# Kernel tuning notes

Hardware: AMD Instinct MI355X
Metric: run time of the kernel (lower is better)

Reference implementation:

```python
import jax, jax.numpy as jnp
import numpy as np

M, N, B, L = 512, 2048, 4, 20
H_DENSITY = 0.02  # Tanner graph sparsity: row weight ~N*p=40, col weight ~M*p=10


def setup_inputs() -> dict:
    key = jax.random.key(0)
    ks = jax.random.split(key, 10)
    H = jax.random.bernoulli(ks[0], H_DENSITY, (M, N)).astype(jnp.float32)
    llrs = jax.random.uniform(ks[1], (N,), jnp.float32)
    syndromes = jax.random.randint(ks[2], (B, M, 1), 0, 2, jnp.int32)
    errors = jax.random.randint(ks[3], (B, N), 0, 2, jnp.int32)
    weights_de = jax.random.uniform(ks[4], (L, M, N), jnp.float32)
    weights_llr = jax.random.uniform(ks[5], (L, N), jnp.float32)
    marg_weights_de = jax.random.uniform(ks[6], (L, M, N), jnp.float32)
    marg_weights_llr = jax.random.uniform(ks[7], (L, N), jnp.float32)
    rhos = jnp.ones((L,), jnp.float32)
    residual_weights = jnp.zeros((L,), jnp.float32)
    return dict(syndromes=syndromes, errors=errors, H=H, llrs=llrs,
                weights_de=weights_de, weights_llr=weights_llr,
                marg_weights_de=marg_weights_de, marg_weights_llr=marg_weights_llr,
                rhos=rhos, residual_weights=residual_weights)


def reference(syndromes, errors, H, llrs, weights_de, weights_llr,
              marg_weights_de, marg_weights_llr, rhos, residual_weights):
    batch = syndromes.shape[0]
    m, n = H.shape
    rhos_norm = jax.nn.softmax(rhos)                       # (L,)
    sign = 1.0 - 2.0 * syndromes.astype(H.dtype)           # (B,m,1): (-1)**syndrome
    err_f = errors.astype(H.dtype)                         # (B,n)
    eps = 1e-6

    def step(msgs_dn, xs):
        w_de, w_llr, mw_de, mw_llr, rho, rw = xs
        # error-node (variable) update: column-sum minus self, masked by H
        msgs_en = (H * (llrs * w_llr)
                   + jnp.sum(msgs_dn * w_de, axis=1, keepdims=True)) * H - msgs_dn
        # detector-node (check) update: tanh-product rule with self-exclusion
        d = jnp.tanh(msgs_en * 0.5)
        d = jnp.where(d == 0, jnp.asarray(1.0, d.dtype), d)
        d = jnp.clip(d, -1.0 + eps, 1.0 - eps)
        row_prod = jnp.prod(d, axis=2, keepdims=True)      # (B,m,1)
        msgs_new = 2.0 * jnp.arctanh(row_prod / d) * (sign * H) + rw * msgs_dn
        # marginal beliefs and weighted BCE loss
        beliefs = jnp.sum(msgs_new * mw_de, axis=1) + llrs * mw_llr   # (B,n)
        loss_b = jnp.sum(jax.nn.softplus(beliefs) - (1.0 - err_f) * beliefs, axis=1)
        return msgs_new, rho * loss_b

    init = jnp.zeros((batch, m, n), H.dtype)
    _, losses = jax.lax.scan(
        step, init,
        (weights_de, weights_llr, marg_weights_de, marg_weights_llr,
         rhos_norm, residual_weights))
    return jnp.sum(losses) / batch
```

## Files before the change

### kernel.cpp

```cpp
#include <hip/hip_runtime.h>

#define MM 512
#define NN 2048
#define BB 4
#define LL 20
#define MAXDEG 128
#define EMAX  24576
#define NT    1024
#define RR    8
#define ROWSB 64
#define SLOTS 4096
#define COLSB 256
#define EPSV  1e-6f

#define WS_ROW_DEG   0
#define WS_ROW_PAD   2048
#define WS_ROW_OFFF  264192
#define WS_ROW_PTR   266240
#define WS_EDGE_CSR  268416
#define WS_WDE_P     366720
#define WS_MWDE_P    2988160
#define WS_COLPART   5609600
#define WS_BELPART   6133888
#define WS_BAR       6658176

__global__ __launch_bounds__(64)
void build_rows(const float* __restrict__ H, int* __restrict__ row_deg,
                int* __restrict__ row_pad, float* __restrict__ row_offf) {
    int i = blockIdx.x, lane = threadIdx.x;
    const float* hrow = H + (size_t)i * NN;
    float v[32];
    #pragma unroll
    for (int c = 0; c < 32; ++c) v[c] = hrow[c * 64 + lane];
    int base = 0;
    #pragma unroll
    for (int c = 0; c < 32; ++c) {
        bool pred = v[c] != 0.0f;
        unsigned long long mask = __ballot(pred);
        int before = __popcll(mask & ((1ull << lane) - 1ull));
        if (pred) {
            int k = base + before;
            if (k < MAXDEG) row_pad[i * MAXDEG + k] = c * 64 + lane;
        }
        base += __popcll(mask);
    }
    if (lane == 0) {
        row_deg[i] = base < MAXDEG ? base : MAXDEG;
        row_offf[i] = powf(1.0f - EPSV, (float)(NN - base));
    }
}

__global__ __launch_bounds__(512)
void scan_rows(const int* __restrict__ row_deg, int* __restrict__ row_ptr) {
    __shared__ int tmp[512];
    int t = threadIdx.x;
    tmp[t] = row_deg[t];
    __syncthreads();
    for (int off = 1; off < 512; off <<= 1) {
        int v = (t >= off) ? tmp[t - off] : 0;
        __syncthreads();
        tmp[t] += v;
        __syncthreads();
    }
    if (t == 0) row_ptr[0] = 0;
    row_ptr[t + 1] = tmp[t];
}

__global__ __launch_bounds__(64)
void fill_csr(const int* __restrict__ row_deg, const int* __restrict__ row_pad,
              const int* __restrict__ row_ptr, unsigned* __restrict__ edge_csr) {
    int i = blockIdx.x, lane = threadIdx.x;
    int deg = row_deg[i], base = row_ptr[i];
    for (int k = lane; k < deg; k += 64)
        edge_csr[base + k] = ((unsigned)i << 16) | (unsigned)row_pad[i * MAXDEG + k];
}

__global__ __launch_bounds__(256)
void gather_weights(const float* __restrict__ w_de, const float* __restrict__ mw_de,
                    const unsigned* __restrict__ edge_csr, const int* __restrict__ row_ptr,
                    float* __restrict__ wde_p, float* __restrict__ mwde_p) {
    int idx = blockIdx.x * 256 + threadIdx.x;
    int l = idx / (RR * SLOTS);
    int rem = idx - l * (RR * SLOTS);
    int r = rem / SLOTS, s = rem - r * SLOTS;
    int e = row_ptr[r * ROWSB] + s;
    if (e < row_ptr[(r + 1) * ROWSB]) {
        unsigned pk = edge_csr[e];
        size_t src = (size_t)l * MM * NN + (size_t)(pk >> 16) * NN + (pk & 0xffffu);
        wde_p[idx]  = w_de[src];
        mwde_p[idx] = mw_de[src];
    } else {
        wde_p[idx]  = 0.0f;
        mwde_p[idx] = 0.0f;
    }
}

__device__ __forceinline__ void grid_barrier(int* ctr) {
    __syncthreads();
    if (threadIdx.x == 0) {
        asm volatile("s_waitcnt vmcnt(0)" ::: "memory");
        __hip_atomic_fetch_add(ctr, 1, __ATOMIC_RELAXED, __HIP_MEMORY_SCOPE_AGENT);
        int it = 0;
        while (__hip_atomic_load(ctr, __ATOMIC_RELAXED, __HIP_MEMORY_SCOPE_AGENT) < RR) {
            __builtin_amdgcn_s_sleep(1);
            if (++it > (1 << 22)) break;
        }
        asm volatile("" ::: "memory");
    }
    __syncthreads();
}

__global__ __launch_bounds__(NT, 4)
void nbp_main(const int* __restrict__ synd, const int* __restrict__ errs,
              const float* __restrict__ llrs,
              const float* __restrict__ w_llr, const float* __restrict__ mw_llr,
              const float* __restrict__ rhos, const float* __restrict__ resw,
              const int* __restrict__ row_ptr, const float* __restrict__ row_offf,
              const unsigned* __restrict__ edge_csr,
              const float* __restrict__ wde_p, const float* __restrict__ mwde_p,
              float* __restrict__ colpart, float* __restrict__ belpart,
              int* __restrict__ bar, float* __restrict__ out) {
    __shared__ float d_sb[SLOTS];
    __shared__ float colsum_s[NN];
    __shared__ float bel_s[NN];
    __shared__ float ncs_s[NN];
    __shared__ float llrs_s[NN];
    __shared__ float rowprod_s[ROWSB];
    __shared__ float rp_coef[ROWSB];
    __shared__ int   rowptr_s[ROWSB + 1];
    __shared__ float rho_n[LL];
    __shared__ float red[16];

    const int blk = blockIdx.x;
    const int b = blk & 3, r = blk >> 2;
    const int i0 = r * ROWSB;
    const int tid = threadIdx.x;
    const int lane = tid & 63, wave = tid >> 6;

    int* bar_b = bar + b * 64;

    if (tid == 0) {
        float mx = -1e30f;
        for (int l = 0; l < LL; ++l) mx = fmaxf(mx, rhos[l]);
        float s = 0.0f;
        for (int l = 0; l < LL; ++l) { float e = __expf(rhos[l] - mx); rho_n[l] = e; s += e; }
        for (int l = 0; l < LL; ++l) rho_n[l] /= s;
    }
    if (tid < ROWSB) {
        int i = i0 + tid;
        rowptr_s[tid] = row_ptr[i];
        rp_coef[tid] = row_offf[i] * (1.0f - 2.0f * (float)synd[b * MM + i]);
    }
    if (tid == ROWSB) rowptr_s[ROWSB] = row_ptr[i0 + ROWSB];
    for (int j = tid; j < NN; j += NT) {
        float lj = llrs[j];
        llrs_s[j] = lj;
        colsum_s[j] = lj * w_llr[j];
    }

    const int e_lo = row_ptr[i0], e_hi = row_ptr[i0 + ROWSB];
    const int cnt = e_hi - e_lo;
    const int s0 = 4 * tid;

    unsigned idx[4];
    float msg[4], d_r[4];
    #pragma unroll
    for (int k = 0; k < 4; ++k) {
        int e = e_lo + s0 + k;
        idx[k] = edge_csr[(s0 + k) < cnt ? e : e_lo] - ((unsigned)i0 << 16);
        msg[k] = 0.0f;
    }
    __syncthreads();

    float loss = 0.0f;

    for (int l = 0; l < LL; ++l) {
        const float rw = resw[l];
        const int par = l & 1;
        float* colpart_b = colpart + ((size_t)par * BB + b) * RR * NN;
        float* belpart_b = belpart + ((size_t)par * BB + b) * RR * NN;

        const float4 mq = *(const float4*)(mwde_p + ((size_t)(l * RR + r) * SLOTS) + s0);
        float4 wq = make_float4(0.f, 0.f, 0.f, 0.f);
        if (l + 1 < LL)
            wq = *(const float4*)(wde_p + ((size_t)((l + 1) * RR + r) * SLOTS) + s0);
        const float mv[4] = {mq.x, mq.y, mq.z, mq.w};
        const float wn[4] = {wq.x, wq.y, wq.z, wq.w};

        #pragma unroll
        for (int k = 0; k < 4; ++k) {
            int j = idx[k] & 0xffffu;
            float en = colsum_s[j] - msg[k];
            float t = __expf(en);
            float d = 1.0f - 2.0f * __builtin_amdgcn_rcpf(t + 1.0f);
            if (d == 0.0f) d = 1.0f;
            d = fminf(fmaxf(d, -1.0f + EPSV), 1.0f - EPSV);
            d_r[k] = d;
        }
        *(float4*)&d_sb[s0] = make_float4(d_r[0], d_r[1], d_r[2], d_r[3]);
        __syncthreads();

        if (tid < 4 * ROWSB) {
            int i = tid >> 2, q = tid & 3;
            int s = rowptr_s[i] - e_lo;
            int deg = rowptr_s[i + 1] - rowptr_s[i];
            float p = 1.0f;
            for (int c = q; c < deg; c += 4) p *= d_sb[s + c];
            p *= __shfl_xor(p, 1);
            p *= __shfl_xor(p, 2);
            if (q == 0) rowprod_s[i] = p * rp_coef[i];
        } else {
            for (int j = tid - 4 * ROWSB; j < NN; j += NT - 4 * ROWSB) {
                bel_s[j] = 0.0f;
                ncs_s[j] = 0.0f;
            }
        }
        __syncthreads();

        #pragma unroll
        for (int k = 0; k < 4; ++k) {
            int il = idx[k] >> 16;
            int j  = idx[k] & 0xffffu;
            float rq = rowprod_s[il] * __builtin_amdgcn_rcpf(d_r[k]);
            float v = __logf(1.0f + rq) - __logf(1.0f - rq) + rw * msg[k];
            msg[k] = v;
            if (s0 + k < cnt) {
                atomicAdd(&bel_s[j], v * mv[k]);
                if (l + 1 < LL) atomicAdd(&ncs_s[j], v * wn[k]);
            }
        }
        __syncthreads();
        for (int j = tid; j < NN; j += NT) {
            __hip_atomic_store(&belpart_b[r * NN + j], bel_s[j],
                               __ATOMIC_RELAXED, __HIP_MEMORY_SCOPE_AGENT);
            __hip_atomic_store(&colpart_b[r * NN + j], ncs_s[j],
                               __ATOMIC_RELAXED, __HIP_MEMORY_SCOPE_AGENT);
        }
        grid_barrier(&bar_b[l]);

        if (tid < COLSB) {
            int j = r * COLSB + tid;
            float bel = llrs_s[j] * mw_llr[l * NN + j];
            float* bp = belpart_b + j;
            #pragma unroll
            for (int r2 = 0; r2 < RR; ++r2)
                bel += __hip_atomic_load(&bp[r2 * NN],
                                         __ATOMIC_RELAXED, __HIP_MEMORY_SCOPE_AGENT);
            float sp = fmaxf(bel, 0.0f) + log1pf(__expf(-fabsf(bel)));
            loss += rho_n[l] * (sp - (1.0f - (float)errs[b * NN + j]) * bel);
        }
        if (l + 1 < LL) {
            const float* wl_next = w_llr + (l + 1) * NN;
            for (int j = tid; j < NN; j += NT) {
                float s = llrs_s[j] * wl_next[j];
                float* cp = colpart_b + j;
                #pragma unroll
                for (int r2 = 0; r2 < RR; ++r2)
                    s += __hip_atomic_load(&cp[r2 * NN],
                                           __ATOMIC_RELAXED, __HIP_MEMORY_SCOPE_AGENT);
                colsum_s[j] = s;
            }
        }
        __syncthreads();
    }

    #pragma unroll
    for (int off = 32; off > 0; off >>= 1) loss += __shfl_down(loss, off);
    if (lane == 0) red[wave] = loss;
    __syncthreads();
    if (wave == 0) {
        float v = (lane < 16) ? red[lane] : 0.0f;
        #pragma unroll
        for (int off = 8; off > 0; off >>= 1) v += __shfl_down(v, off);
        if (lane == 0) atomicAdd(out, v * 0.25f);
    }
}

extern "C" void kernel_launch(void* const* d_in, const int* in_sizes, int n_in,
                              void* d_out, int out_size, void* d_ws, size_t ws_size,
                              hipStream_t stream) {
    const int*   synd  = (const int*)  d_in[0];
    const int*   errs  = (const int*)  d_in[1];
    const float* H     = (const float*)d_in[2];
    const float* llrs  = (const float*)d_in[3];
    const float* w_de  = (const float*)d_in[4];
    const float* w_llr = (const float*)d_in[5];
    const float* mw_de = (const float*)d_in[6];
    const float* mw_llr= (const float*)d_in[7];
    const float* rhos  = (const float*)d_in[8];
    const float* resw  = (const float*)d_in[9];

    char* ws = (char*)d_ws;
    int*      row_deg  = (int*)     (ws + WS_ROW_DEG);
    int*      row_pad  = (int*)     (ws + WS_ROW_PAD);
    float*    row_offf = (float*)   (ws + WS_ROW_OFFF);
    int*      row_ptr  = (int*)     (ws + WS_ROW_PTR);
    unsigned* edge_csr = (unsigned*)(ws + WS_EDGE_CSR);
    float*    wde_p    = (float*)   (ws + WS_WDE_P);
    float*    mwde_p   = (float*)   (ws + WS_MWDE_P);
    float*    colpart  = (float*)   (ws + WS_COLPART);
    float*    belpart  = (float*)   (ws + WS_BELPART);
    int*      bar      = (int*)     (ws + WS_BAR);
    float*    out      = (float*)d_out;

    hipMemsetAsync(bar, 0, BB * 64 * sizeof(int), stream);
    hipMemsetAsync(d_out, 0, sizeof(float), stream);

    build_rows<<<MM, 64, 0, stream>>>(H, row_deg, row_pad, row_offf);
    scan_rows<<<1, 512, 0, stream>>>(row_deg, row_ptr);
    fill_csr<<<MM, 64, 0, stream>>>(row_deg, row_pad, row_ptr, edge_csr);
    gather_weights<<<(LL * RR * SLOTS) / 256, 256, 0, stream>>>(w_de, mw_de, edge_csr,
                                                                row_ptr, wde_p, mwde_p);
    nbp_main<<<BB * RR, NT, 0, stream>>>(synd, errs, llrs, w_llr, mw_llr, rhos, resw,
                                         row_ptr, row_offf, edge_csr, wde_p, mwde_p,
                                         colpart, belpart, bar, out);
}
```

Before: 424.7 us.

## Partition edges by column slices instead of row blocks to shrink cross-block exchange

Each of the 8 blocks per batch now owns a 256-column slice of the edges instead of a 64-row slice. Column sums and beliefs become block-local, so the only cross-block exchange per layer is 512 partial row products per slice, down from two full 2048-wide column partial arrays. The setup now needs count, scan and fill passes per slice, and rows are reduced serially per thread. The grid barrier moves to between the row-product phase and the message update.

```diff
diff --git a/kernel.cpp b/kernel.cpp
--- a/kernel.cpp
+++ b/kernel.cpp
@@ -5,24 +5,22 @@
 #define BB 4
 #define LL 20
 #define MAXDEG 128
-#define EMAX  24576
 #define NT    1024
 #define RR    8
-#define ROWSB 64
+#define COLSB 256
 #define SLOTS 4096
-#define COLSB 256
 #define EPSV  1e-6f
 
 #define WS_ROW_DEG   0
 #define WS_ROW_PAD   2048
 #define WS_ROW_OFFF  264192
-#define WS_ROW_PTR   266240
-#define WS_EDGE_CSR  268416
-#define WS_WDE_P     366720
-#define WS_MWDE_P    2988160
-#define WS_COLPART   5609600
-#define WS_BELPART   6133888
-#define WS_BAR       6658176
+#define WS_DEG_RB    266240
+#define WS_RPTR_RB   282624
+#define WS_EDGE_CS   299040
+#define WS_WDE_P     430112
+#define WS_MWDE_P    3051552
+#define WS_PP        5672992
+#define WS_BAR       5804064
 
 __global__ __launch_bounds__(64)
 void build_rows(const float* __restrict__ H, int* __restrict__ row_deg,
@@ -51,10 +49,26 @@
 }
 
 __global__ __launch_bounds__(512)
-void scan_rows(const int* __restrict__ row_deg, int* __restrict__ row_ptr) {
+void count_slices(const int* __restrict__ row_deg, const int* __restrict__ row_pad,
+                  int* __restrict__ deg_rb) {
+    int i = threadIdx.x;
+    int deg = row_deg[i];
+    int cnt[RR];
+    #pragma unroll
+    for (int r = 0; r < RR; ++r) cnt[r] = 0;
+    for (int k = 0; k < deg; ++k) {
+        int c = row_pad[i * MAXDEG + k];
+        cnt[c >> 8]++;
+    }
+    #pragma unroll
+    for (int r = 0; r < RR; ++r) deg_rb[r * MM + i] = cnt[r];
+}
+
+__global__ __launch_bounds__(512)
+void scan_slices(const int* __restrict__ deg_rb, int* __restrict__ rptr_rb) {
     __shared__ int tmp[512];
-    int t = threadIdx.x;
-    tmp[t] = row_deg[t];
+    int r = blockIdx.x, t = threadIdx.x;
+    tmp[t] = deg_rb[r * MM + t];
     __syncthreads();
     for (int off = 1; off < 512; off <<= 1) {
         int v = (t >= off) ? tmp[t - off] : 0;
@@ -62,30 +76,39 @@
         tmp[t] += v;
         __syncthreads();
     }
-    if (t == 0) row_ptr[0] = 0;
-    row_ptr[t + 1] = tmp[t];
-}
-
-__global__ __launch_bounds__(64)
-void fill_csr(const int* __restrict__ row_deg, const int* __restrict__ row_pad,
-              const int* __restrict__ row_ptr, unsigned* __restrict__ edge_csr) {
-    int i = blockIdx.x, lane = threadIdx.x;
-    int deg = row_deg[i], base = row_ptr[i];
-    for (int k = lane; k < deg; k += 64)
-        edge_csr[base + k] = ((unsigned)i << 16) | (unsigned)row_pad[i * MAXDEG + k];
+    if (t == 0) rptr_rb[r * 513] = 0;
+    rptr_rb[r * 513 + t + 1] = tmp[t];
+}
+
+__global__ __launch_bounds__(512)
+void fill_cs(const int* __restrict__ row_deg, const int* __restrict__ row_pad,
+             const int* __restrict__ rptr_rb, unsigned* __restrict__ edge_cs) {
+    int i = threadIdx.x;
+    int deg = row_deg[i];
+    int cnt[RR];
+    #pragma unroll
+    for (int r = 0; r < RR; ++r) cnt[r] = 0;
+    for (int k = 0; k < deg; ++k) {
+        int c = row_pad[i * MAXDEG + k];
+        int r = c >> 8;
+        int pos = rptr_rb[r * 513 + i] + cnt[r]++;
+        if (pos < SLOTS)
+            edge_cs[r * SLOTS + pos] = ((unsigned)i << 16) | (unsigned)c;
+    }
 }
 
 __global__ __launch_bounds__(256)
 void gather_weights(const float* __restrict__ w_de, const float* __restrict__ mw_de,
-                    const unsigned* __restrict__ edge_csr, const int* __restrict__ row_ptr,
+                    const unsigned* __restrict__ edge_cs, const int* __restrict__ rptr_rb,
                     float* __restrict__ wde_p, float* __restrict__ mwde_p) {
     int idx = blockIdx.x * 256 + threadIdx.x;
     int l = idx / (RR * SLOTS);
     int rem = idx - l * (RR * SLOTS);
     int r = rem / SLOTS, s = rem - r * SLOTS;
-    int e = row_ptr[r * ROWSB] + s;
-    if (e < row_ptr[(r + 1) * ROWSB]) {
-        unsigned pk = edge_csr[e];
+    int tot = rptr_rb[r * 513 + MM];
+    if (tot > SLOTS) tot = SLOTS;
+    if (s < tot) {
+        unsigned pk = edge_cs[r * SLOTS + s];
         size_t src = (size_t)l * MM * NN + (size_t)(pk >> 16) * NN + (pk & 0xffffu);
         wde_p[idx]  = w_de[src];
         mwde_p[idx] = mw_de[src];
@@ -115,25 +138,25 @@
               const float* __restrict__ llrs,
               const float* __restrict__ w_llr, const float* __restrict__ mw_llr,
               const float* __restrict__ rhos, const float* __restrict__ resw,
-              const int* __restrict__ row_ptr, const float* __restrict__ row_offf,
-              const unsigned* __restrict__ edge_csr,
+              const int* __restrict__ rptr_rb, const float* __restrict__ row_offf,
+              const unsigned* __restrict__ edge_cs,
               const float* __restrict__ wde_p, const float* __restrict__ mwde_p,
-              float* __restrict__ colpart, float* __restrict__ belpart,
-              int* __restrict__ bar, float* __restrict__ out) {
+              float* __restrict__ pp, int* __restrict__ bar,
+              float* __restrict__ out) {
     __shared__ float d_sb[SLOTS];
-    __shared__ float colsum_s[NN];
-    __shared__ float bel_s[NN];
-    __shared__ float ncs_s[NN];
-    __shared__ float llrs_s[NN];
-    __shared__ float rowprod_s[ROWSB];
-    __shared__ float rp_coef[ROWSB];
-    __shared__ int   rowptr_s[ROWSB + 1];
+    __shared__ float colsum_s[COLSB];
+    __shared__ float bel_s[COLSB];
+    __shared__ float ncs_s[COLSB];
+    __shared__ float llrs_s[COLSB];
+    __shared__ float ef_s[COLSB];
+    __shared__ float rowprod_s[MM];
+    __shared__ float rp_coef[MM];
+    __shared__ int   rowptr_s[MM + 1];
     __shared__ float rho_n[LL];
     __shared__ float red[16];
 
     const int blk = blockIdx.x;
     const int b = blk & 3, r = blk >> 2;
-    const int i0 = r * ROWSB;
     const int tid = threadIdx.x;
     const int lane = tid & 63, wave = tid >> 6;
 
@@ -146,28 +169,31 @@
         for (int l = 0; l < LL; ++l) { float e = __expf(rhos[l] - mx); rho_n[l] = e; s += e; }
         for (int l = 0; l < LL; ++l) rho_n[l] /= s;
     }
-    if (tid < ROWSB) {
-        int i = i0 + tid;
-        rowptr_s[tid] = row_ptr[i];
-        rp_coef[tid] = row_offf[i] * (1.0f - 2.0f * (float)synd[b * MM + i]);
-    }
-    if (tid == ROWSB) rowptr_s[ROWSB] = row_ptr[i0 + ROWSB];
-    for (int j = tid; j < NN; j += NT) {
+    if (tid < MM) {
+        rowptr_s[tid] = rptr_rb[r * 513 + tid];
+        rp_coef[tid] = row_offf[tid] * (1.0f - 2.0f * (float)synd[b * MM + tid]);
+    }
+    if (tid == MM) rowptr_s[MM] = rptr_rb[r * 513 + MM];
+    if (tid < COLSB) {
+        int j = r * COLSB + tid;
         float lj = llrs[j];
-        llrs_s[j] = lj;
-        colsum_s[j] = lj * w_llr[j];
-    }
-
-    const int e_lo = row_ptr[i0], e_hi = row_ptr[i0 + ROWSB];
-    const int cnt = e_hi - e_lo;
+        llrs_s[tid] = lj;
+        colsum_s[tid] = lj * w_llr[j];
+        ef_s[tid] = 1.0f - (float)errs[b * NN + j];
+        bel_s[tid] = 0.0f;
+        ncs_s[tid] = 0.0f;
+    }
+
+    int cnt = rptr_rb[r * 513 + MM];
+    if (cnt > SLOTS) cnt = SLOTS;
     const int s0 = 4 * tid;
 
     unsigned idx[4];
     float msg[4], d_r[4];
     #pragma unroll
     for (int k = 0; k < 4; ++k) {
-        int e = e_lo + s0 + k;
-        idx[k] = edge_csr[(s0 + k) < cnt ? e : e_lo] - ((unsigned)i0 << 16);
+        int e = r * SLOTS + s0 + k;
+        idx[k] = edge_cs[(s0 + k) < cnt ? e : r * SLOTS];
         msg[k] = 0.0f;
     }
     __syncthreads();
@@ -177,8 +203,7 @@
     for (int l = 0; l < LL; ++l) {
         const float rw = resw[l];
         const int par = l & 1;
-        float* colpart_b = colpart + ((size_t)par * BB + b) * RR * NN;
-        float* belpart_b = belpart + ((size_t)par * BB + b) * RR * NN;
+        float* pp_b = pp + ((size_t)par * BB + b) * RR * MM;
 
         const float4 mq = *(const float4*)(mwde_p + ((size_t)(l * RR + r) * SLOTS) + s0);
         float4 wq = make_float4(0.f, 0.f, 0.f, 0.f);
@@ -189,8 +214,8 @@
 
         #pragma unroll
         for (int k = 0; k < 4; ++k) {
-            int j = idx[k] & 0xffffu;
-            float en = colsum_s[j] - msg[k];
+            int jl = idx[k] & 255u;
+            float en = colsum_s[jl] - msg[k];
             float t = __expf(en);
             float d = 1.0f - 2.0f * __builtin_amdgcn_rcpf(t + 1.0f);
             if (d == 0.0f) d = 1.0f;
@@ -200,65 +225,49 @@
         *(float4*)&d_sb[s0] = make_float4(d_r[0], d_r[1], d_r[2], d_r[3]);
         __syncthreads();
 
-        if (tid < 4 * ROWSB) {
-            int i = tid >> 2, q = tid & 3;
-            int s = rowptr_s[i] - e_lo;
-            int deg = rowptr_s[i + 1] - rowptr_s[i];
+        if (tid < MM) {
+            int lo = rowptr_s[tid], hi = rowptr_s[tid + 1];
+            if (hi > SLOTS) hi = SLOTS;
             float p = 1.0f;
-            for (int c = q; c < deg; c += 4) p *= d_sb[s + c];
-            p *= __shfl_xor(p, 1);
-            p *= __shfl_xor(p, 2);
-            if (q == 0) rowprod_s[i] = p * rp_coef[i];
-        } else {
-            for (int j = tid - 4 * ROWSB; j < NN; j += NT - 4 * ROWSB) {
-                bel_s[j] = 0.0f;
-                ncs_s[j] = 0.0f;
-            }
+            for (int s = lo; s < hi; ++s) p *= d_sb[s];
+            __hip_atomic_store(&pp_b[r * MM + tid], p,
+                               __ATOMIC_RELAXED, __HIP_MEMORY_SCOPE_AGENT);
+        }
+        grid_barrier(&bar_b[l]);
+
+        if (tid < MM) {
+            float p = rp_coef[tid];
+            #pragma unroll
+            for (int r2 = 0; r2 < RR; ++r2)
+                p *= __hip_atomic_load(&pp_b[r2 * MM + tid],
+                                       __ATOMIC_RELAXED, __HIP_MEMORY_SCOPE_AGENT);
+            rowprod_s[tid] = p;
         }
         __syncthreads();
 
         #pragma unroll
         for (int k = 0; k < 4; ++k) {
             int il = idx[k] >> 16;
-            int j  = idx[k] & 0xffffu;
+            int jl = idx[k] & 255u;
             float rq = rowprod_s[il] * __builtin_amdgcn_rcpf(d_r[k]);
             float v = __logf(1.0f + rq) - __logf(1.0f - rq) + rw * msg[k];
             msg[k] = v;
             if (s0 + k < cnt) {
-                atomicAdd(&bel_s[j], v * mv[k]);
-                if (l + 1 < LL) atomicAdd(&ncs_s[j], v * wn[k]);
+                atomicAdd(&bel_s[jl], v * mv[k]);
+                if (l + 1 < LL) atomicAdd(&ncs_s[jl], v * wn[k]);
             }
         }
         __syncthreads();
-        for (int j = tid; j < NN; j += NT) {
-            __hip_atomic_store(&belpart_b[r * NN + j], bel_s[j],
-                               __ATOMIC_RELAXED, __HIP_MEMORY_SCOPE_AGENT);
-            __hip_atomic_store(&colpart_b[r * NN + j], ncs_s[j],
-                               __ATOMIC_RELAXED, __HIP_MEMORY_SCOPE_AGENT);
-        }
-        grid_barrier(&bar_b[l]);
 
         if (tid < COLSB) {
             int j = r * COLSB + tid;
-            float bel = llrs_s[j] * mw_llr[l * NN + j];
-            float* bp = belpart_b + j;
-            #pragma unroll
-            for (int r2 = 0; r2 < RR; ++r2)
-                bel += __hip_atomic_load(&bp[r2 * NN],
-                                         __ATOMIC_RELAXED, __HIP_MEMORY_SCOPE_AGENT);
+            float bel = llrs_s[tid] * mw_llr[l * NN + j] + bel_s[tid];
+            bel_s[tid] = 0.0f;
             float sp = fmaxf(bel, 0.0f) + log1pf(__expf(-fabsf(bel)));
-            loss += rho_n[l] * (sp - (1.0f - (float)errs[b * NN + j]) * bel);
-        }
-        if (l + 1 < LL) {
-            const float* wl_next = w_llr + (l + 1) * NN;
-            for (int j = tid; j < NN; j += NT) {
-                float s = llrs_s[j] * wl_next[j];
-                float* cp = colpart_b + j;
-                #pragma unroll
-                for (int r2 = 0; r2 < RR; ++r2)
-                    s += __hip_atomic_load(&cp[r2 * NN],
-                                           __ATOMIC_RELAXED, __HIP_MEMORY_SCOPE_AGENT);
-                colsum_s[j] = s;
+            loss += rho_n[l] * (sp - ef_s[tid] * bel);
+            if (l + 1 < LL) {
+                colsum_s[tid] = llrs_s[tid] * w_llr[(l + 1) * NN + j] + ncs_s[tid];
+                ncs_s[tid] = 0.0f;
             }
         }
         __syncthreads();
@@ -294,12 +303,12 @@
     int*      row_deg  = (int*)     (ws + WS_ROW_DEG);
     int*      row_pad  = (int*)     (ws + WS_ROW_PAD);
     float*    row_offf = (float*)   (ws + WS_ROW_OFFF);
-    int*      row_ptr  = (int*)     (ws + WS_ROW_PTR);
-    unsigned* edge_csr = (unsigned*)(ws + WS_EDGE_CSR);
+    int*      deg_rb   = (int*)     (ws + WS_DEG_RB);
+    int*      rptr_rb  = (int*)     (ws + WS_RPTR_RB);
+    unsigned* edge_cs  = (unsigned*)(ws + WS_EDGE_CS);
     float*    wde_p    = (float*)   (ws + WS_WDE_P);
     float*    mwde_p   = (float*)   (ws + WS_MWDE_P);
-    float*    colpart  = (float*)   (ws + WS_COLPART);
-    float*    belpart  = (float*)   (ws + WS_BELPART);
+    float*    pp       = (float*)   (ws + WS_PP);
     int*      bar      = (int*)     (ws + WS_BAR);
     float*    out      = (float*)d_out;
 
@@ -307,11 +316,12 @@
     hipMemsetAsync(d_out, 0, sizeof(float), stream);
 
     build_rows<<<MM, 64, 0, stream>>>(H, row_deg, row_pad, row_offf);
-    scan_rows<<<1, 512, 0, stream>>>(row_deg, row_ptr);
-    fill_csr<<<MM, 64, 0, stream>>>(row_deg, row_pad, row_ptr, edge_csr);
-    gather_weights<<<(LL * RR * SLOTS) / 256, 256, 0, stream>>>(w_de, mw_de, edge_csr,
-                                                                row_ptr, wde_p, mwde_p);
+    count_slices<<<1, 512, 0, stream>>>(row_deg, row_pad, deg_rb);
+    scan_slices<<<RR, 512, 0, stream>>>(deg_rb, rptr_rb);
+    fill_cs<<<1, 512, 0, stream>>>(row_deg, row_pad, rptr_rb, edge_cs);
+    gather_weights<<<(LL * RR * SLOTS) / 256, 256, 0, stream>>>(w_de, mw_de, edge_cs,
+                                                                rptr_rb, wde_p, mwde_p);
     nbp_main<<<BB * RR, NT, 0, stream>>>(synd, errs, llrs, w_llr, mw_llr, rhos, resw,
-                                         row_ptr, row_offf, edge_csr, wde_p, mwde_p,
-                                         colpart, belpart, bar, out);
-}
+                                         rptr_rb, row_offf, edge_cs, wde_p, mwde_p,
+                                         pp, bar, out);
+}
```

New measurement: 454.8 us. +7.1%, slower.
